# Kernel optimization log

Measured on AMD Instinct MI355X. Metric: run time of the kernel, lower is better.

## Reference

```python
import jax, jax.numpy as jnp
import numpy as np

ITERS = 8
LAMBDA0 = 0.01
PAD = 1.0
LR = 1.0
EPS = 1e-12


def _sobel_grads(fmap):
    # kornia spatial_gradient: normalized 3x3 sobel (/8), replicate padding. fmap: C,H,W
    kx = jnp.array([[-1., 0., 1.], [-2., 0., 2.], [-1., 0., 1.]], fmap.dtype) / 8.0
    k = jnp.stack([kx, kx.T])[:, None]                       # 2,1,3,3 (OIHW)
    f = jnp.pad(fmap, ((0, 0), (1, 1), (1, 1)), mode='edge')[:, None]  # C,1,H+2,W+2
    g = jax.lax.conv_general_dilated(f, k, (1, 1), 'VALID')  # C,2,H,W
    return g[:, 0], g[:, 1]


def _bilinear(tensor, pts):
    # grid_sample bilinear, align_corners=True, at pixel coords. tensor: C,H,W; pts: N,2 (x,y) -> N,C
    c, h, w = tensor.shape
    x, y = pts[:, 0], pts[:, 1]
    x0 = jnp.clip(jnp.floor(x), 0, w - 1)
    y0 = jnp.clip(jnp.floor(y), 0, h - 1)
    x1 = jnp.clip(x0 + 1, 0, w - 1)
    y1 = jnp.clip(y0 + 1, 0, h - 1)
    wx, wy = x - x0, y - y0
    x0i, x1i = x0.astype(jnp.int32), x1.astype(jnp.int32)
    y0i, y1i = y0.astype(jnp.int32), y1.astype(jnp.int32)
    v00 = tensor[:, y0i, x0i]
    v01 = tensor[:, y0i, x1i]
    v10 = tensor[:, y1i, x0i]
    v11 = tensor[:, y1i, x1i]
    out = (v00 * (1 - wx) * (1 - wy) + v01 * wx * (1 - wy)
           + v10 * (1 - wx) * wy + v11 * wx * wy)
    return out.T


def _skew(v):
    x, y, z = v[..., 0], v[..., 1], v[..., 2]
    o = jnp.zeros_like(x)
    return jnp.stack([o, -z, y, z, o, -x, -y, x, o], -1).reshape(v.shape[:-1] + (3, 3))


def _so3exp(w):
    theta = jnp.linalg.norm(w)
    small = theta < 1e-7
    th = jnp.where(small, 1.0, theta)
    A = jnp.where(small, 1.0, jnp.sin(th) / th)
    B = jnp.where(small, 0.5, (1.0 - jnp.cos(th)) / th ** 2)
    W = _skew(w)
    return jnp.eye(3, dtype=w.dtype) + A * W + B * (W @ W)


def _normalize(x):
    return x / jnp.maximum(jnp.linalg.norm(x, axis=-1, keepdims=True), EPS)


def _pnp(p3D, feature_ref, feature_query, K, R_init, t_init):
    C, H, W = feature_query.shape
    gx, gy = _sobel_grads(feature_query)
    fref = _normalize(feature_ref)
    fx, fy, cx, cy = K[0, 0], K[1, 1], K[0, 2], K[1, 2]
    f_scale = jnp.stack([fx, fy])
    c_off = jnp.stack([cx, cy])

    def project(R, t):
        p3q = p3D @ R.T + t
        pn = p3q[:, :2] / p3q[:, 2:3]
        return p3q, pn, pn * f_scale + c_off

    def in_image(p2):
        return ((p2[:, 0] >= PAD) & (p2[:, 0] < W - PAD)
                & (p2[:, 1] >= PAD) & (p2[:, 1] < H - PAD))

    def masked_cost(p2, vf):
        f = _normalize(_bilinear(feature_query, p2))
        cost = ((f - fref) ** 2).sum(-1)
        return (cost * vf).sum() / vf.sum()

    R, t = R_init, t_init
    lam = jnp.asarray(LAMBDA0, p3D.dtype)
    jacobi = None
    cost_best = None
    p2D_init = None

    for i in range(ITERS):
        p3q, pn, p2 = project(R, t)
        if i == 0:
            p2D_init = jax.lax.stop_gradient(p2)
        vf = in_image(p2).astype(p3D.dtype)  # mask-weight == gather of valid pts

        f_raw = _bilinear(feature_query, p2)  # N,C
        norm = jnp.maximum(jnp.linalg.norm(f_raw, axis=-1, keepdims=True), EPS)
        f = f_raw / norm
        error = f - fref
        if i == 0:
            cost_best = (((error ** 2).sum(-1)) * vf).sum() / vf.sum()

        # Jacobian chain: J = J_f_p2 @ J_p2_pn @ J_pn_p3 @ J_p3_T   -> N,C,6
        x_, y_, d = p3q[:, 0], p3q[:, 1], p3q[:, 2]
        z = jnp.zeros_like(d)
        Jpn = jnp.stack([1 / d, z, -x_ / d ** 2,
                         z, 1 / d, -y_ / d ** 2], -1).reshape(-1, 2, 3)
        Jpn = Jpn * f_scale[None, :, None]  # fold in J_p2_pn = diag(fx,fy)
        Jp3T = jnp.concatenate(
            [jnp.broadcast_to(jnp.eye(3, dtype=p3D.dtype), p3q.shape[:-1] + (3, 3)),
             -_skew(p3q)], -1)  # N,3,6
        J26 = Jpn @ Jp3T       # N,2,6

        Jf = jnp.stack([_bilinear(gx, p2), _bilinear(gy, p2)], -1)  # N,C,2
        # normalize-feat Jacobian (I - f f^T)/||f_raw||, fused (no NxCxC)
        proj = jnp.einsum('nc,nck->nk', f, Jf)
        Jf = (Jf - f[:, :, None] * proj[:, None, :]) / norm[:, :, None]

        J = Jf @ J26  # N,C,6
        if i == 0:
            jacobi = 1.0 / (1.0 + jnp.linalg.norm(J * vf[:, None, None], axis=(0, 1)))
        J = J * jacobi

        Grad = jnp.einsum('ncj,nc,n->j', J, error, vf)
        Hess = jnp.einsum('nci,ncj,n->ij', J, J, vf)

        damp = jnp.diag(jnp.diagonal(Hess) + 1e-9) * lam  # LM damping
        delta = -LR * jnp.linalg.solve(Hess + damp, Grad)
        delta = delta * jacobi
        dt, dw = delta[:3], delta[3:6]
        dr = _so3exp(dw)
        R_new, t_new = dr @ R, dr @ t + dt

        _, _, p2_new = project(R_new, t_new)
        vf_new = in_image(p2_new).astype(p3D.dtype)
        cost_new = masked_cost(p2_new, vf_new)

        accept = cost_new <= cost_best
        lam = jnp.clip(lam * jnp.where(accept, 0.1, 10.0), 1e-8, 1e4)
        R = jnp.where(accept, R_new, R)
        t = jnp.where(accept, t_new, t)
        cost_best = jnp.where(accept, cost_new, cost_best)

    p3D_sg = jax.lax.stop_gradient(p3D)
    pf = p3D_sg @ R.T + t
    p2f = (pf[:, :2] / pf[:, 2:3]) * f_scale + c_off
    f_i = _normalize(_bilinear(feature_query, p2D_init))
    f_f = _normalize(_bilinear(feature_query, p2f))
    cost_init = ((fref - f_i) ** 2).sum(-1)
    cost_final = ((fref - f_f) ** 2).sum(-1)
    nan = jnp.asarray(jnp.nan, cost_init.dtype)
    cost_init = jnp.where(in_image(p2D_init), cost_init, nan)
    cost_final = jnp.where(in_image(p2f), cost_final, nan)
    return R, t, cost_init, cost_final


def setup_inputs() -> dict:
    N, C, H, W = 10000, 128, 512, 512
    key = jax.random.key(0)
    ks = jax.random.split(key, 4)
    xy = jax.random.uniform(ks[0], (N, 2), jnp.float32, -2.0, 2.0)
    z = jax.random.uniform(ks[1], (N, 1), jnp.float32, 4.0, 10.0)
    p3D = jnp.concatenate([xy, z], -1)
    feature_query = jax.random.normal(ks[2], (C, H, W), jnp.float32) * 0.5
    feature_ref = jax.random.normal(ks[3], (N, C), jnp.float32)
    K = jnp.array([[500., 0., 256.], [0., 500., 256.], [0., 0., 1.]], jnp.float32)
    R_init = _so3exp(jnp.array([0.01, -0.02, 0.015], jnp.float32))
    t_init = jnp.array([0.05, -0.03, 0.10], jnp.float32)
    return {"p3D": p3D, "feature_ref": feature_ref, "feature_query": feature_query,
            "K": K, "R_init": R_init, "t_init": t_init}


def reference(p3D, feature_ref, feature_query, K, R_init, t_init):
    return _pnp(p3D, feature_ref, feature_query, K, R_init, t_init)
```

## Files before the change

### kernel.cpp

```cpp
#include <hip/hip_runtime.h>
#include <hip/hip_fp16.h>
#include <math.h>

#define HW_ (512*512)
#define CSTRIDE 32

typedef float vf4 __attribute__((ext_vector_type(4)));

__device__ __forceinline__ float wred(float v){
#pragma unroll
  for (int o = 32; o > 0; o >>= 1) v += __shfl_xor(v, o, 64);
  return v;
}

template<bool TR>
__device__ __forceinline__ float2 tap(const void* __restrict__ f, int y, int x, int c0){
  if (TR){
    const __half2* p = (const __half2*)f + (((size_t)((y << 9) + x)) << 6) + (c0 >> 1);
    return __half22float2(*p);
  } else {
    const float* ff = (const float*)f;
    int base = (y << 9) + x;
    float2 r;
    r.x = ff[(size_t)c0 * HW_ + base];
    r.y = ff[(size_t)(c0 + 1) * HW_ + base];
    return r;
  }
}

__device__ __forceinline__ void fgrad(const float P[16], float w00, float w01, float w10, float w11,
                                      float& f, float& gx, float& gy){
  f = w00*P[5] + w01*P[6] + w10*P[9] + w11*P[10];
  float gx11 = (P[2]  + 2.f*P[6]  + P[10] - P[0] - 2.f*P[4]  - P[8] ) * 0.125f;
  float gx12 = (P[3]  + 2.f*P[7]  + P[11] - P[1] - 2.f*P[5]  - P[9] ) * 0.125f;
  float gx21 = (P[6]  + 2.f*P[10] + P[14] - P[4] - 2.f*P[8]  - P[12]) * 0.125f;
  float gx22 = (P[7]  + 2.f*P[11] + P[15] - P[5] - 2.f*P[9]  - P[13]) * 0.125f;
  gx = w00*gx11 + w01*gx12 + w10*gx21 + w11*gx22;
  float gy11 = (P[8]  + 2.f*P[9]  + P[10] - P[0] - 2.f*P[1]  - P[2] ) * 0.125f;
  float gy12 = (P[9]  + 2.f*P[10] + P[11] - P[1] - 2.f*P[2]  - P[3] ) * 0.125f;
  float gy21 = (P[12] + 2.f*P[13] + P[14] - P[4] - 2.f*P[5]  - P[6] ) * 0.125f;
  float gy22 = (P[13] + 2.f*P[14] + P[15] - P[5] - 2.f*P[6]  - P[7] ) * 0.125f;
  gy = w00*gy11 + w01*gy12 + w10*gy21 + w11*gy22;
}

template<bool TR>
__device__ __forceinline__ float cost_point_raw(const void* __restrict__ fmap,
                                                const float* __restrict__ fref,
                                                int n, float px, float py, int lane){
  int c0 = 2 * lane;
  float x0f = fminf(fmaxf(floorf(px), 0.f), 511.f);
  float y0f = fminf(fmaxf(floorf(py), 0.f), 511.f);
  int x0 = (int)x0f, y0 = (int)y0f;
  int x1 = min(x0 + 1, 511), y1 = min(y0 + 1, 511);
  float wx = px - x0f, wy = py - y0f;
  float w00 = (1.f-wx)*(1.f-wy), w01 = wx*(1.f-wy), w10 = (1.f-wx)*wy, w11 = wx*wy;
  float2 a = tap<TR>(fmap, y0, x0, c0), b = tap<TR>(fmap, y0, x1, c0);
  float2 c = tap<TR>(fmap, y1, x0, c0), d = tap<TR>(fmap, y1, x1, c0);
  float f0 = w00*a.x + w01*b.x + w10*c.x + w11*d.x;
  float f1 = w00*a.y + w01*b.y + w10*c.y + w11*d.y;
  const float2 fr = *(const float2*)(fref + (size_t)n*128 + c0);
  float Sff  = wred(f0*f0 + f1*f1);
  float Sffr = wred(f0*fr.x + f1*fr.y);
  float Sfr  = wred(fr.x*fr.x + fr.y*fr.y);
  float inv = 1.f / fmaxf(sqrtf(Sff), 1e-12f);
  float irn = 1.f / fmaxf(sqrtf(Sfr), 1e-12f);
  return Sff*inv*inv - 2.f*Sffr*inv*irn + Sfr*irn*irn;
}

__global__ __launch_bounds__(512) void transpose_kernel(const float* __restrict__ fq,
                                                        __half* __restrict__ ftr,
                                                        double* __restrict__ cur2){
  __shared__ __half tile[256 * 128];
  int t = threadIdx.x;
  if (blockIdx.x == 0 && t < 32) cur2[t * CSTRIDE] = 0.0;
  int sb = blockIdx.x << 8;
  int l = t & 63, r = t >> 6;
  int px0 = l << 2;
#pragma unroll
  for (int p = 0; p < 16; p++){
    int ch = p * 8 + r;
    vf4 v = __builtin_nontemporal_load((const vf4*)(fq + (size_t)ch * HW_ + sb + px0));
#pragma unroll
    for (int j = 0; j < 4; j++){
      int px = px0 + j;
      tile[px * 128 + (ch ^ (px & 0x78))] = __float2half(v[j]);
    }
  }
  __syncthreads();
#pragma unroll
  for (int p = 0; p < 8; p++){
    int px = p * 32 + (t >> 4);
    int c8 = (t & 15) << 3;
    int cs = c8 ^ (px & 0x78);
    uint4 v = *(const uint4*)&tile[px * 128 + cs];
    *(uint4*)(ftr + ((size_t)(sb + px) << 7) + c8) = v;
  }
}

__global__ void init_kernel(double* __restrict__ cur2){
  if (threadIdx.x < 32) cur2[threadIdx.x * CSTRIDE] = 0.0;
}

template<bool TR>
__device__ __forceinline__ bool gather_pt(
    const float* __restrict__ p3D, const float* __restrict__ fref,
    const void* __restrict__ fmap, const float* Rl, const float* Tl,
    float fx, float fy, float cx, float cy,
    int n, int lane, float s[10], float& X, float& Y, float& D)
{
  float PX = p3D[3*n], PY = p3D[3*n+1], PZ = p3D[3*n+2];
  X = Rl[0]*PX + Rl[1]*PY + Rl[2]*PZ + Tl[0];
  Y = Rl[3]*PX + Rl[4]*PY + Rl[5]*PZ + Tl[1];
  D = Rl[6]*PX + Rl[7]*PY + Rl[8]*PZ + Tl[2];
  float px = X / D * fx + cx;
  float py = Y / D * fy + cy;
  if (!(px >= 1.f && px < 511.f && py >= 1.f && py < 511.f)) return false;
  int c0 = 2 * lane;
  float x0f = fminf(fmaxf(floorf(px), 0.f), 511.f);
  float y0f = fminf(fmaxf(floorf(py), 0.f), 511.f);
  int x0 = (int)x0f, y0 = (int)y0f;
  int x1 = min(x0 + 1, 511), y1 = min(y0 + 1, 511);
  float wx = px - x0f, wy = py - y0f;
  int xs[4] = {max(x0-1,0), x0, x1, min(x1+1,511)};
  int ys[4] = {max(y0-1,0), y0, y1, min(y1+1,511)};
  float Pa[16], Pb[16];
#pragma unroll
  for (int rr = 0; rr < 4; rr++)
#pragma unroll
    for (int sc = 0; sc < 4; sc++){
      float2 v = tap<TR>(fmap, ys[rr], xs[sc], c0);
      Pa[rr*4+sc] = v.x; Pb[rr*4+sc] = v.y;
    }
  float w00 = (1.f-wx)*(1.f-wy), w01 = wx*(1.f-wy), w10 = (1.f-wx)*wy, w11 = wx*wy;
  float f0, gx0, gy0, f1, gx1, gy1;
  fgrad(Pa, w00, w01, w10, w11, f0, gx0, gy0);
  fgrad(Pb, w00, w01, w10, w11, f1, gx1, gy1);
  const float2 fr = *(const float2*)(fref + (size_t)n*128 + c0);
  s[0] = f0*f0 + f1*f1;
  s[1] = f0*fr.x + f1*fr.y;
  s[2] = fr.x*fr.x + fr.y*fr.y;
  s[3] = f0*gx0 + f1*gx1;
  s[4] = f0*gy0 + f1*gy1;
  s[5] = gx0*fr.x + gx1*fr.y;
  s[6] = gy0*fr.x + gy1*fr.y;
  s[7] = gx0*gx0 + gx1*gx1;
  s[8] = gx0*gy0 + gx1*gy1;
  s[9] = gy0*gy0 + gy1*gy1;
  return true;
}

__device__ __forceinline__ float slot_val(const float s[10], float X, float Y, float D,
                                          float fx, float fy, int lane, int li, int lj,
                                          float& se2)
{
  float inv = 1.f / fmaxf(sqrtf(s[0]), 1e-12f);
  float irn = 1.f / fmaxf(sqrtf(s[2]), 1e-12f);
  float inv2 = inv*inv, inv3 = inv2*inv, inv4 = inv2*inv2;
  float Sffr = s[1]*irn, Sgxfr = s[5]*irn, Sgyfr = s[6]*irn, Sfr = s[2]*irn*irn;
  se2 = s[0]*inv2 - 2.f*Sffr*inv + Sfr;
  float gex = s[3]*inv2 - Sgxfr*inv - s[3]*s[0]*inv4 + s[3]*Sffr*inv3;
  float gey = s[4]*inv2 - Sgyfr*inv - s[4]*s[0]*inv4 + s[4]*Sffr*inv3;
  float sxx = s[7]*inv2 - s[3]*s[3]*inv4;
  float sxy = s[8]*inv2 - s[3]*s[4]*inv4;
  float syy = s[9]*inv2 - s[4]*s[4]*inv4;
  float invD = 1.f / D;
  float rx = X * invD, ry = Y * invD;
  float A[6] = {fx*invD, 0.f, -fx*rx*invD, -fx*rx*ry, fx*(1.f+rx*rx), -fx*ry};
  float B[6] = {0.f, fy*invD, -fy*ry*invD, -fy*(1.f+ry*ry), fy*rx*ry, fy*rx};
  float val = 0.f;
  if (lane < 6)        val = A[lane]*gex + B[lane]*gey;
  else if (lane < 27)  val = A[li]*A[lj]*sxx + (A[li]*B[lj] + A[lj]*B[li])*sxy + B[li]*B[lj]*syy;
  else if (lane == 27) val = se2;
  else if (lane == 28) val = 1.f;
  return val;
}

template<bool TR>
__global__ __launch_bounds__(512) void eval_kernel(
    const float* __restrict__ p3D, const float* __restrict__ fref,
    const void* __restrict__ fmap, const float* __restrict__ Km,
    const float* __restrict__ Rm, const float* __restrict__ tm,
    double* __restrict__ cur2, float* __restrict__ cost_out, int N)
{
  int t = threadIdx.x;
  int lane = t & 63;
  int wv = t >> 6;
  int gw = blockIdx.x * 8 + wv;
  int n0 = gw * 2, n1 = n0 + 1;
  float fx = Km[0], fy = Km[4], cx = Km[2], cy = Km[5];
  float Rl[9], Tl[3];
#pragma unroll
  for (int i = 0; i < 9; i++) Rl[i] = Rm[i];
#pragma unroll
  for (int i = 0; i < 3; i++) Tl[i] = tm[i];
  int li = 0, lj = 0;
  {
    const int pi_[21] = {0,0,0,0,0,0,1,1,1,1,1,2,2,2,2,3,3,3,4,4,5};
    const int pj_[21] = {0,1,2,3,4,5,1,2,3,4,5,2,3,4,5,3,4,5,4,5,5};
    if (lane >= 6 && lane < 27){ li = pi_[lane-6]; lj = pj_[lane-6]; }
  }
  float sA[10], sB[10];
  float XA=0, YA=0, DA=1, XB=0, YB=0, DB=1;
  bool vA = false, vB = false;
  if (n0 < N) vA = gather_pt<TR>(p3D, fref, fmap, Rl, Tl, fx, fy, cx, cy, n0, lane, sA, XA, YA, DA);
  if (n1 < N) vB = gather_pt<TR>(p3D, fref, fmap, Rl, Tl, fx, fy, cx, cy, n1, lane, sB, XB, YB, DB);
  if (vA){
#pragma unroll
    for (int i = 0; i < 10; i++) sA[i] = wred(sA[i]);
  }
  if (vB){
#pragma unroll
    for (int i = 0; i < 10; i++) sB[i] = wred(sB[i]);
  }
  double acc = 0.0;
  float se2A = 0.f, se2B = 0.f;
  if (vA) acc += (double)slot_val(sA, XA, YA, DA, fx, fy, lane, li, lj, se2A);
  if (vB) acc += (double)slot_val(sB, XB, YB, DB, fx, fy, lane, li, lj, se2B);
  if (cost_out && lane == 0){
    const float nanv = __int_as_float(0x7fc00000);
    if (n0 < N) cost_out[n0] = vA ? se2A : nanv;
    if (n1 < N) cost_out[n1] = vB ? se2B : nanv;
  }
  __shared__ double red[8][32];
  if (lane < 32) red[wv][lane] = acc;
  __syncthreads();
  if (t < 32){
    double ssum = 0.0;
#pragma unroll
    for (int i = 0; i < 8; i++) ssum += red[i][t];
    if (ssum != 0.0) atomicAdd(&cur2[t * CSTRIDE], ssum);
  }
}

template<bool TR>
__global__ __launch_bounds__(512) void cost_kernel(
    const float* __restrict__ p3D, const float* __restrict__ fref,
    const void* __restrict__ fmap, const float* __restrict__ Km,
    const float* __restrict__ Rm, const float* __restrict__ tm,
    double* __restrict__ cur2, int N)
{
  int t = threadIdx.x;
  int lane = t & 63;
  int wv = t >> 6;
  int gw = blockIdx.x * 8 + wv;
  int n0 = gw * 2, n1 = n0 + 1;
  float fx = Km[0], fy = Km[4], cx = Km[2], cy = Km[5];
  float Rl[9], Tl[3];
#pragma unroll
  for (int i = 0; i < 9; i++) Rl[i] = Rm[i];
#pragma unroll
  for (int i = 0; i < 3; i++) Tl[i] = tm[i];
  double accc = 0.0, accn = 0.0;
#pragma unroll
  for (int q = 0; q < 2; q++){
    int n = q ? n1 : n0;
    if (n >= N) continue;
    float PX = p3D[3*n], PY = p3D[3*n+1], PZ = p3D[3*n+2];
    float X = Rl[0]*PX + Rl[1]*PY + Rl[2]*PZ + Tl[0];
    float Y = Rl[3]*PX + Rl[4]*PY + Rl[5]*PZ + Tl[1];
    float D = Rl[6]*PX + Rl[7]*PY + Rl[8]*PZ + Tl[2];
    float px = X / D * fx + cx, py = Y / D * fy + cy;
    if (px >= 1.f && px < 511.f && py >= 1.f && py < 511.f){
      float cp = cost_point_raw<TR>(fmap, fref, n, px, py, lane);
      accc += (double)cp; accn += 1.0;
    }
  }
  double acc = (lane == 27) ? accc : ((lane == 28) ? accn : 0.0);
  __shared__ double red[8][32];
  if (lane < 32) red[wv][lane] = acc;
  __syncthreads();
  if (t < 32){
    double ssum = 0.0;
#pragma unroll
    for (int i = 0; i < 8; i++) ssum += red[i][t];
    if (ssum != 0.0) atomicAdd(&cur2[t * CSTRIDE], ssum);
  }
}

__device__ void solve_step(const double* __restrict__ cur, float* __restrict__ state){
  const int pi_[21] = {0,0,0,0,0,0,1,1,1,1,1,2,2,2,2,3,3,3,4,4,5};
  const int pj_[21] = {0,1,2,3,4,5,1,2,3,4,5,2,3,4,5,3,4,5,4,5,5};
  double rg[6]; for (int i = 0; i < 6; i++) rg[i] = cur[i];
  double rh[6][6];
  for (int k = 0; k < 21; k++){ rh[pi_[k]][pj_[k]] = cur[6+k]; rh[pj_[k]][pi_[k]] = cur[6+k]; }
  float jac[6];
  for (int j = 0; j < 6; j++) jac[j] = state[24+j];
  double lam = (double)state[30];
  double H[6][7];
  for (int i = 0; i < 6; i++)
    for (int j = 0; j < 6; j++) H[i][j] = (double)jac[i] * (double)jac[j] * rh[i][j];
  for (int i = 0; i < 6; i++) H[i][i] += (H[i][i] + 1e-9) * lam;
  for (int i = 0; i < 6; i++) H[i][6] = -((double)jac[i] * rg[i]);
  for (int k = 0; k < 6; k++){
    int p = k; double mx = fabs(H[k][k]);
    for (int r = k+1; r < 6; r++) if (fabs(H[r][k]) > mx){ mx = fabs(H[r][k]); p = r; }
    if (p != k) for (int c = k; c < 7; c++){ double tmp = H[k][c]; H[k][c] = H[p][c]; H[p][c] = tmp; }
    double inv = 1.0 / H[k][k];
    for (int r = k+1; r < 6; r++){
      double m = H[r][k] * inv;
      for (int c = k; c < 7; c++) H[r][c] -= m * H[k][c];
    }
  }
  double d[6];
  for (int i = 5; i >= 0; i--){
    double sx = H[i][6];
    for (int c = i+1; c < 6; c++) sx -= H[i][c] * d[c];
    d[i] = sx / H[i][i];
  }
  for (int j = 0; j < 6; j++) d[j] *= (double)jac[j];
  double wx = d[3], wy = d[4], wz = d[5];
  double th2 = wx*wx + wy*wy + wz*wz, th = sqrt(th2);
  double Aa, Bb;
  if (th < 1e-7){ Aa = 1.0; Bb = 0.5; } else { Aa = sin(th)/th; Bb = (1.0 - cos(th))/th2; }
  double W[3][3] = {{0,-wz,wy},{wz,0,-wx},{-wy,wx,0}};
  double W2[3][3];
  for (int i = 0; i < 3; i++) for (int j = 0; j < 3; j++){
    double q = 0; for (int k = 0; k < 3; k++) q += W[i][k]*W[k][j]; W2[i][j] = q;
  }
  double dr[3][3];
  for (int i = 0; i < 3; i++) for (int j = 0; j < 3; j++)
    dr[i][j] = (i == j ? 1.0 : 0.0) + Aa*W[i][j] + Bb*W2[i][j];
  double Rc[3][3], tc[3];
  for (int i = 0; i < 3; i++){ tc[i] = state[9+i]; for (int j = 0; j < 3; j++) Rc[i][j] = state[i*3+j]; }
  for (int i = 0; i < 3; i++){
    for (int j = 0; j < 3; j++){
      double q = 0; for (int k = 0; k < 3; k++) q += dr[i][k]*Rc[k][j];
      state[12 + i*3 + j] = (float)q;
    }
    double q = 0; for (int k = 0; k < 3; k++) q += dr[i][k]*tc[k];
    state[21 + i] = (float)(q + d[i]);
  }
}

__global__ void update_kernel(double* __restrict__ cur2, float* __restrict__ state,
                              double* __restrict__ cur,
                              const float* __restrict__ Rin, const float* __restrict__ tin,
                              int iter)
{
  if (threadIdx.x != 0) return;
  double tot[32];
  for (int i = 0; i < 32; i++){ tot[i] = cur2[i * CSTRIDE]; cur2[i * CSTRIDE] = 0.0; }
  if (iter < 0){
    for (int i = 0; i < 9; i++) state[i] = Rin[i];
    for (int i = 0; i < 3; i++) state[9+i] = tin[i];
    state[30] = 0.01f;
    const int diag_k[6] = {0, 6, 11, 15, 18, 20};
    for (int j = 0; j < 6; j++)
      state[24+j] = 1.0f / (1.0f + (float)sqrt(tot[6 + diag_k[j]]));
    state[31] = (float)(tot[27] / tot[28]);
    for (int k = 0; k < 32; k++) cur[k] = tot[k];
    solve_step(cur, state);
  } else {
    float cn = (float)(tot[27] / tot[28]);
    bool acpt = (cn <= state[31]);
    float lam = state[30] * (acpt ? 0.1f : 10.f);
    state[30] = fminf(fmaxf(lam, 1e-8f), 1e4f);
    if (acpt){
      for (int i = 0; i < 12; i++) state[i] = state[12+i];
      state[31] = cn;
      for (int k = 0; k < 32; k++) cur[k] = tot[k];
    }
    if (iter < 7) solve_step(cur, state);
  }
}

template<bool TR>
__global__ __launch_bounds__(256) void final_kernel(
    const float* __restrict__ p3D, const float* __restrict__ fref,
    const void* __restrict__ fmap, const float* __restrict__ Km,
    const float* __restrict__ state, float* __restrict__ out, int N)
{
  if (blockIdx.x == 0 && threadIdx.x < 12) out[threadIdx.x] = state[threadIdx.x];
  int lane = threadIdx.x & 63;
  int n = blockIdx.x * 4 + (threadIdx.x >> 6);
  if (n >= N) return;
  float fx = Km[0], fy = Km[4], cx = Km[2], cy = Km[5];
  float PX = p3D[3*n], PY = p3D[3*n+1], PZ = p3D[3*n+2];
  float X = state[0]*PX + state[1]*PY + state[2]*PZ + state[9];
  float Y = state[3]*PX + state[4]*PY + state[5]*PZ + state[10];
  float D = state[6]*PX + state[7]*PY + state[8]*PZ + state[11];
  float px = X / D * fx + cx, py = Y / D * fy + cy;
  bool vf = (px >= 1.f && px < 511.f && py >= 1.f && py < 511.f);
  float cf = __int_as_float(0x7fc00000);
  if (vf) cf = cost_point_raw<TR>(fmap, fref, n, px, py, lane);
  if (lane == 0) out[12 + N + n] = cf;
}

extern "C" void kernel_launch(void* const* d_in, const int* in_sizes, int n_in,
                              void* d_out, int out_size, void* d_ws, size_t ws_size,
                              hipStream_t stream)
{
  const float* p3D  = (const float*)d_in[0];
  const float* fref = (const float*)d_in[1];
  const float* fq   = (const float*)d_in[2];
  const float* Km   = (const float*)d_in[3];
  const float* Rin  = (const float*)d_in[4];
  const float* tin  = (const float*)d_in[5];
  float* out = (float*)d_out;
  int N = in_sizes[0] / 3;
  int NEB   = (N + 15) / 16;
  int NBLK4 = (N + 3) / 4;

  char* w = (char*)d_ws;
  float*  state = (float*)w;
  double* cur   = (double*)(w + 256);
  double* cur2  = (double*)(w + 512);
  size_t ftr_off = (512 + 32 * CSTRIDE * 8 + 255) & ~(size_t)255;
  __half* ftr = (__half*)(w + ftr_off);
  size_t need = ftr_off + (size_t)HW_ * 128 * 2;
  bool tr = (ws_size >= need);

  if (tr) transpose_kernel<<<HW_/256, 512, 0, stream>>>(fq, ftr, cur2);
  else    init_kernel<<<1, 64, 0, stream>>>(cur2);
  const void* fmap = tr ? (const void*)ftr : (const void*)fq;

  if (tr) eval_kernel<true ><<<NEB, 512, 0, stream>>>(p3D, fref, fmap, Km, Rin, tin, cur2, out + 12, N);
  else    eval_kernel<false><<<NEB, 512, 0, stream>>>(p3D, fref, fmap, Km, Rin, tin, cur2, out + 12, N);
  update_kernel<<<1, 64, 0, stream>>>(cur2, state, cur, Rin, tin, -1);

  for (int it = 0; it < 7; it++){
    if (tr) eval_kernel<true ><<<NEB, 512, 0, stream>>>(p3D, fref, fmap, Km, state + 12, state + 21, cur2, nullptr, N);
    else    eval_kernel<false><<<NEB, 512, 0, stream>>>(p3D, fref, fmap, Km, state + 12, state + 21, cur2, nullptr, N);
    update_kernel<<<1, 64, 0, stream>>>(cur2, state, cur, Rin, tin, it);
  }
  if (tr) cost_kernel<true ><<<NEB, 512, 0, stream>>>(p3D, fref, fmap, Km, state + 12, state + 21, cur2, N);
  else    cost_kernel<false><<<NEB, 512, 0, stream>>>(p3D, fref, fmap, Km, state + 12, state + 21, cur2, N);
  update_kernel<<<1, 64, 0, stream>>>(cur2, state, cur, Rin, tin, 7);

  if (tr) final_kernel<true ><<<NBLK4, 256, 0, stream>>>(p3D, fref, fmap, Km, state, out, N);
  else    final_kernel<false><<<NBLK4, 256, 0, stream>>>(p3D, fref, fmap, Km, state, out, N);
}
```

Before: 485.5 us.

## Cache per-point costs across LM iterations and restructure eval into persistent grid-stride

Per-point costs from each trial pose are kept in a workspace buffer and copied into the final-cost output when the update accepts a step. This removes the final kernel's re-gather of the feature map, which now only copies cached values. Eval and cost kernels switch to a fixed 1024-block grid-stride loop with 256-thread blocks and one point per wave per pass. The atomic accumulators are spread over 8 slots per quantity and summed in the update kernel. The sobel/bilinear gather is also restructured to stream one row of taps at a time with folded weights, which lowers register pressure at the cost of more logic coupling the kernels through state[32].

```diff
diff --git a/kernel.cpp b/kernel.cpp
--- a/kernel.cpp
+++ b/kernel.cpp
@@ -3,7 +3,6 @@
 #include <math.h>
 
 #define HW_ (512*512)
-#define CSTRIDE 32
 
 typedef float vf4 __attribute__((ext_vector_type(4)));
 
@@ -26,21 +25,6 @@
     r.y = ff[(size_t)(c0 + 1) * HW_ + base];
     return r;
   }
-}
-
-__device__ __forceinline__ void fgrad(const float P[16], float w00, float w01, float w10, float w11,
-                                      float& f, float& gx, float& gy){
-  f = w00*P[5] + w01*P[6] + w10*P[9] + w11*P[10];
-  float gx11 = (P[2]  + 2.f*P[6]  + P[10] - P[0] - 2.f*P[4]  - P[8] ) * 0.125f;
-  float gx12 = (P[3]  + 2.f*P[7]  + P[11] - P[1] - 2.f*P[5]  - P[9] ) * 0.125f;
-  float gx21 = (P[6]  + 2.f*P[10] + P[14] - P[4] - 2.f*P[8]  - P[12]) * 0.125f;
-  float gx22 = (P[7]  + 2.f*P[11] + P[15] - P[5] - 2.f*P[9]  - P[13]) * 0.125f;
-  gx = w00*gx11 + w01*gx12 + w10*gx21 + w11*gx22;
-  float gy11 = (P[8]  + 2.f*P[9]  + P[10] - P[0] - 2.f*P[1]  - P[2] ) * 0.125f;
-  float gy12 = (P[9]  + 2.f*P[10] + P[11] - P[1] - 2.f*P[2]  - P[3] ) * 0.125f;
-  float gy21 = (P[12] + 2.f*P[13] + P[14] - P[4] - 2.f*P[5]  - P[6] ) * 0.125f;
-  float gy22 = (P[13] + 2.f*P[14] + P[15] - P[5] - 2.f*P[6]  - P[7] ) * 0.125f;
-  gy = w00*gy11 + w01*gy12 + w10*gy21 + w11*gy22;
 }
 
 template<bool TR>
@@ -72,7 +56,7 @@
                                                         double* __restrict__ cur2){
   __shared__ __half tile[256 * 128];
   int t = threadIdx.x;
-  if (blockIdx.x == 0 && t < 32) cur2[t * CSTRIDE] = 0.0;
+  if (blockIdx.x == 0 && t < 256) cur2[t] = 0.0;
   int sb = blockIdx.x << 8;
   int l = t & 63, r = t >> 6;
   int px0 = l << 2;
@@ -98,7 +82,7 @@
 }
 
 __global__ void init_kernel(double* __restrict__ cur2){
-  if (threadIdx.x < 32) cur2[threadIdx.x * CSTRIDE] = 0.0;
+  if (threadIdx.x < 256) cur2[threadIdx.x] = 0.0;
 }
 
 template<bool TR>
@@ -121,20 +105,42 @@
   int x0 = (int)x0f, y0 = (int)y0f;
   int x1 = min(x0 + 1, 511), y1 = min(y0 + 1, 511);
   float wx = px - x0f, wy = py - y0f;
-  int xs[4] = {max(x0-1,0), x0, x1, min(x1+1,511)};
-  int ys[4] = {max(y0-1,0), y0, y1, min(y1+1,511)};
-  float Pa[16], Pb[16];
-#pragma unroll
-  for (int rr = 0; rr < 4; rr++)
-#pragma unroll
-    for (int sc = 0; sc < 4; sc++){
-      float2 v = tap<TR>(fmap, ys[rr], xs[sc], c0);
-      Pa[rr*4+sc] = v.x; Pb[rr*4+sc] = v.y;
-    }
-  float w00 = (1.f-wx)*(1.f-wy), w01 = wx*(1.f-wy), w10 = (1.f-wx)*wy, w11 = wx*wy;
-  float f0, gx0, gy0, f1, gx1, gy1;
-  fgrad(Pa, w00, w01, w10, w11, f0, gx0, gy0);
-  fgrad(Pb, w00, w01, w10, w11, f1, gx1, gy1);
+  int xs0 = max(x0-1,0), xs3 = min(x1+1,511);
+  int ys0 = max(y0-1,0), ys3 = min(y1+1,511);
+  float ea = (1.f-wx)*(1.f-wy), eb = wx*(1.f-wy), ec = (1.f-wx)*wy, ed = wx*wy;
+  float a8 = 0.125f*ea, b8 = 0.125f*eb, c8 = 0.125f*ec, d8 = 0.125f*ed;
+  float gL1 = 2.f*a8 + c8, gR1 = 2.f*b8 + d8;
+  float gL2 = a8 + 2.f*c8, gR2 = b8 + 2.f*d8;
+  float ya0 = a8, ya1 = 2.f*a8 + b8, ya2 = a8 + 2.f*b8, ya3 = b8;
+  float yc0 = c8, yc1 = 2.f*c8 + d8, yc2 = c8 + 2.f*d8, yc3 = d8;
+  float f0=0.f, f1=0.f, gx0=0.f, gx1=0.f, gy0=0.f, gy1=0.f;
+  float2 t0, t1, t2, t3;
+  t0 = tap<TR>(fmap, ys0, xs0, c0); t1 = tap<TR>(fmap, ys0, x0, c0);
+  t2 = tap<TR>(fmap, ys0, x1,  c0); t3 = tap<TR>(fmap, ys0, xs3, c0);
+  gx0 += a8*(t2.x-t0.x) + b8*(t3.x-t1.x);
+  gx1 += a8*(t2.y-t0.y) + b8*(t3.y-t1.y);
+  gy0 -= ya0*t0.x + ya1*t1.x + ya2*t2.x + ya3*t3.x;
+  gy1 -= ya0*t0.y + ya1*t1.y + ya2*t2.y + ya3*t3.y;
+  t0 = tap<TR>(fmap, y0, xs0, c0); t1 = tap<TR>(fmap, y0, x0, c0);
+  t2 = tap<TR>(fmap, y0, x1,  c0); t3 = tap<TR>(fmap, y0, xs3, c0);
+  gx0 += gL1*(t2.x-t0.x) + gR1*(t3.x-t1.x);
+  gx1 += gL1*(t2.y-t0.y) + gR1*(t3.y-t1.y);
+  gy0 -= yc0*t0.x + yc1*t1.x + yc2*t2.x + yc3*t3.x;
+  gy1 -= yc0*t0.y + yc1*t1.y + yc2*t2.y + yc3*t3.y;
+  f0 += ea*t1.x + eb*t2.x;  f1 += ea*t1.y + eb*t2.y;
+  t0 = tap<TR>(fmap, y1, xs0, c0); t1 = tap<TR>(fmap, y1, x0, c0);
+  t2 = tap<TR>(fmap, y1, x1,  c0); t3 = tap<TR>(fmap, y1, xs3, c0);
+  gx0 += gL2*(t2.x-t0.x) + gR2*(t3.x-t1.x);
+  gx1 += gL2*(t2.y-t0.y) + gR2*(t3.y-t1.y);
+  gy0 += ya0*t0.x + ya1*t1.x + ya2*t2.x + ya3*t3.x;
+  gy1 += ya0*t0.y + ya1*t1.y + ya2*t2.y + ya3*t3.y;
+  f0 += ec*t1.x + ed*t2.x;  f1 += ec*t1.y + ed*t2.y;
+  t0 = tap<TR>(fmap, ys3, xs0, c0); t1 = tap<TR>(fmap, ys3, x0, c0);
+  t2 = tap<TR>(fmap, ys3, x1,  c0); t3 = tap<TR>(fmap, ys3, xs3, c0);
+  gx0 += c8*(t2.x-t0.x) + d8*(t3.x-t1.x);
+  gx1 += c8*(t2.y-t0.y) + d8*(t3.y-t1.y);
+  gy0 += yc0*t0.x + yc1*t1.x + yc2*t2.x + yc3*t3.x;
+  gy1 += yc0*t0.y + yc1*t1.y + yc2*t2.y + yc3*t3.y;
   const float2 fr = *(const float2*)(fref + (size_t)n*128 + c0);
   s[0] = f0*f0 + f1*f1;
   s[1] = f0*fr.x + f1*fr.y;
@@ -176,17 +182,21 @@
 }
 
 template<bool TR>
-__global__ __launch_bounds__(512) void eval_kernel(
+__global__ __launch_bounds__(256) void eval_kernel(
     const float* __restrict__ p3D, const float* __restrict__ fref,
     const void* __restrict__ fmap, const float* __restrict__ Km,
     const float* __restrict__ Rm, const float* __restrict__ tm,
-    double* __restrict__ cur2, float* __restrict__ cost_out, int N)
-{
-  int t = threadIdx.x;
-  int lane = t & 63;
-  int wv = t >> 6;
-  int gw = blockIdx.x * 8 + wv;
-  int n0 = gw * 2, n1 = n0 + 1;
+    const float* __restrict__ state, double* __restrict__ cur2,
+    float* __restrict__ costT, float* __restrict__ costF,
+    float* __restrict__ costI, int N, int mode)
+{
+  int t = threadIdx.x, lane = t & 63, wv = t >> 6;
+  int gw = blockIdx.x * 4 + wv;
+  int nw = (gridDim.x * blockDim.x) >> 6;
+  if (mode == 1 && state[32] != 0.f){
+    int nn = gw + lane * nw;
+    if (lane < 4 && nn < N) costF[nn] = costT[nn];
+  }
   float fx = Km[0], fy = Km[4], cx = Km[2], cy = Km[5];
   float Rl[9], Tl[3];
 #pragma unroll
@@ -199,81 +209,73 @@
     const int pj_[21] = {0,1,2,3,4,5,1,2,3,4,5,2,3,4,5,3,4,5,4,5,5};
     if (lane >= 6 && lane < 27){ li = pi_[lane-6]; lj = pj_[lane-6]; }
   }
-  float sA[10], sB[10];
-  float XA=0, YA=0, DA=1, XB=0, YB=0, DB=1;
-  bool vA = false, vB = false;
-  if (n0 < N) vA = gather_pt<TR>(p3D, fref, fmap, Rl, Tl, fx, fy, cx, cy, n0, lane, sA, XA, YA, DA);
-  if (n1 < N) vB = gather_pt<TR>(p3D, fref, fmap, Rl, Tl, fx, fy, cx, cy, n1, lane, sB, XB, YB, DB);
-  if (vA){
-#pragma unroll
-    for (int i = 0; i < 10; i++) sA[i] = wred(sA[i]);
-  }
-  if (vB){
-#pragma unroll
-    for (int i = 0; i < 10; i++) sB[i] = wred(sB[i]);
-  }
+  const float nanv = __int_as_float(0x7fc00000);
   double acc = 0.0;
-  float se2A = 0.f, se2B = 0.f;
-  if (vA) acc += (double)slot_val(sA, XA, YA, DA, fx, fy, lane, li, lj, se2A);
-  if (vB) acc += (double)slot_val(sB, XB, YB, DB, fx, fy, lane, li, lj, se2B);
-  if (cost_out && lane == 0){
-    const float nanv = __int_as_float(0x7fc00000);
-    if (n0 < N) cost_out[n0] = vA ? se2A : nanv;
-    if (n1 < N) cost_out[n1] = vB ? se2B : nanv;
-  }
-  __shared__ double red[8][32];
+  for (int n = gw; n < N; n += nw){
+    float s[10], X, Y, D;
+    bool v = gather_pt<TR>(p3D, fref, fmap, Rl, Tl, fx, fy, cx, cy, n, lane, s, X, Y, D);
+    float se2 = 0.f;
+    if (v){
+#pragma unroll
+      for (int i = 0; i < 10; i++) s[i] = wred(s[i]);
+      acc += (double)slot_val(s, X, Y, D, fx, fy, lane, li, lj, se2);
+    }
+    if (lane == 0){
+      float cv = v ? se2 : nanv;
+      if (mode == 0){ costI[n] = cv; costF[n] = cv; }
+      else costT[n] = cv;
+    }
+  }
+  __shared__ double red[4][32];
   if (lane < 32) red[wv][lane] = acc;
   __syncthreads();
   if (t < 32){
-    double ssum = 0.0;
-#pragma unroll
-    for (int i = 0; i < 8; i++) ssum += red[i][t];
-    if (ssum != 0.0) atomicAdd(&cur2[t * CSTRIDE], ssum);
+    double ssum = red[0][t] + red[1][t] + red[2][t] + red[3][t];
+    if (ssum != 0.0) atomicAdd(&cur2[t*8 + (blockIdx.x & 7)], ssum);
   }
 }
 
 template<bool TR>
-__global__ __launch_bounds__(512) void cost_kernel(
+__global__ __launch_bounds__(256) void cost_kernel(
     const float* __restrict__ p3D, const float* __restrict__ fref,
     const void* __restrict__ fmap, const float* __restrict__ Km,
     const float* __restrict__ Rm, const float* __restrict__ tm,
-    double* __restrict__ cur2, int N)
-{
-  int t = threadIdx.x;
-  int lane = t & 63;
-  int wv = t >> 6;
-  int gw = blockIdx.x * 8 + wv;
-  int n0 = gw * 2, n1 = n0 + 1;
+    const float* __restrict__ state, double* __restrict__ cur2,
+    float* __restrict__ costT, float* __restrict__ costF, int N)
+{
+  int t = threadIdx.x, lane = t & 63, wv = t >> 6;
+  int gw = blockIdx.x * 4 + wv;
+  int nw = (gridDim.x * blockDim.x) >> 6;
+  if (state[32] != 0.f){
+    int nn = gw + lane * nw;
+    if (lane < 4 && nn < N) costF[nn] = costT[nn];
+  }
   float fx = Km[0], fy = Km[4], cx = Km[2], cy = Km[5];
   float Rl[9], Tl[3];
 #pragma unroll
   for (int i = 0; i < 9; i++) Rl[i] = Rm[i];
 #pragma unroll
   for (int i = 0; i < 3; i++) Tl[i] = tm[i];
+  const float nanv = __int_as_float(0x7fc00000);
   double accc = 0.0, accn = 0.0;
-#pragma unroll
-  for (int q = 0; q < 2; q++){
-    int n = q ? n1 : n0;
-    if (n >= N) continue;
+  for (int n = gw; n < N; n += nw){
     float PX = p3D[3*n], PY = p3D[3*n+1], PZ = p3D[3*n+2];
     float X = Rl[0]*PX + Rl[1]*PY + Rl[2]*PZ + Tl[0];
     float Y = Rl[3]*PX + Rl[4]*PY + Rl[5]*PZ + Tl[1];
     float D = Rl[6]*PX + Rl[7]*PY + Rl[8]*PZ + Tl[2];
     float px = X / D * fx + cx, py = Y / D * fy + cy;
-    if (px >= 1.f && px < 511.f && py >= 1.f && py < 511.f){
-      float cp = cost_point_raw<TR>(fmap, fref, n, px, py, lane);
-      accc += (double)cp; accn += 1.0;
-    }
+    bool v = (px >= 1.f && px < 511.f && py >= 1.f && py < 511.f);
+    float cp = 0.f;
+    if (v){ cp = cost_point_raw<TR>(fmap, fref, n, px, py, lane); accc += (double)cp; accn += 1.0; }
+    if (lane == 0) costT[n] = v ? cp : nanv;
   }
   double acc = (lane == 27) ? accc : ((lane == 28) ? accn : 0.0);
-  __shared__ double red[8][32];
+  __shared__ double red[4][32];
   if (lane < 32) red[wv][lane] = acc;
   __syncthreads();
   if (t < 32){
-    double ssum = 0.0;
-#pragma unroll
-    for (int i = 0; i < 8; i++) ssum += red[i][t];
-    if (ssum != 0.0) atomicAdd(&cur2[t * CSTRIDE], ssum);
+    double ssum = red[0][t] + red[1][t] + red[2][t] + red[3][t];
+    if (ssum != 0.0) atomicAdd(&cur2[t*8 + (blockIdx.x & 7)], ssum);
   }
 }
 
@@ -337,13 +339,21 @@
                               const float* __restrict__ Rin, const float* __restrict__ tin,
                               int iter)
 {
-  if (threadIdx.x != 0) return;
-  double tot[32];
-  for (int i = 0; i < 32; i++){ tot[i] = cur2[i * CSTRIDE]; cur2[i * CSTRIDE] = 0.0; }
+  __shared__ double tot[32];
+  int t = threadIdx.x;
+  if (t < 32){
+    double s = 0.0;
+#pragma unroll
+    for (int k = 0; k < 8; k++){ s += cur2[t*8 + k]; cur2[t*8 + k] = 0.0; }
+    tot[t] = s;
+  }
+  __syncthreads();
+  if (t != 0) return;
   if (iter < 0){
     for (int i = 0; i < 9; i++) state[i] = Rin[i];
     for (int i = 0; i < 3; i++) state[9+i] = tin[i];
     state[30] = 0.01f;
+    state[32] = 0.f;
     const int diag_k[6] = {0, 6, 11, 15, 18, 20};
     for (int j = 0; j < 6; j++)
       state[24+j] = 1.0f / (1.0f + (float)sqrt(tot[6 + diag_k[j]]));
@@ -355,6 +365,7 @@
     bool acpt = (cn <= state[31]);
     float lam = state[30] * (acpt ? 0.1f : 10.f);
     state[30] = fminf(fmaxf(lam, 1e-8f), 1e4f);
+    state[32] = acpt ? 1.f : 0.f;
     if (acpt){
       for (int i = 0; i < 12; i++) state[i] = state[12+i];
       state[31] = cn;
@@ -364,26 +375,16 @@
   }
 }
 
-template<bool TR>
-__global__ __launch_bounds__(256) void final_kernel(
-    const float* __restrict__ p3D, const float* __restrict__ fref,
-    const void* __restrict__ fmap, const float* __restrict__ Km,
-    const float* __restrict__ state, float* __restrict__ out, int N)
-{
-  if (blockIdx.x == 0 && threadIdx.x < 12) out[threadIdx.x] = state[threadIdx.x];
-  int lane = threadIdx.x & 63;
-  int n = blockIdx.x * 4 + (threadIdx.x >> 6);
-  if (n >= N) return;
-  float fx = Km[0], fy = Km[4], cx = Km[2], cy = Km[5];
-  float PX = p3D[3*n], PY = p3D[3*n+1], PZ = p3D[3*n+2];
-  float X = state[0]*PX + state[1]*PY + state[2]*PZ + state[9];
-  float Y = state[3]*PX + state[4]*PY + state[5]*PZ + state[10];
-  float D = state[6]*PX + state[7]*PY + state[8]*PZ + state[11];
-  float px = X / D * fx + cx, py = Y / D * fy + cy;
-  bool vf = (px >= 1.f && px < 511.f && py >= 1.f && py < 511.f);
-  float cf = __int_as_float(0x7fc00000);
-  if (vf) cf = cost_point_raw<TR>(fmap, fref, n, px, py, lane);
-  if (lane == 0) out[12 + N + n] = cf;
+__global__ __launch_bounds__(256) void final_kernel(const float* __restrict__ state,
+                                                    const float* __restrict__ costT,
+                                                    float* __restrict__ out, int N)
+{
+  int g = blockIdx.x * blockDim.x + threadIdx.x;
+  if (g < 12) out[g] = state[g];
+  if (state[32] != 0.f){
+    int stride = gridDim.x * blockDim.x;
+    for (int n = g; n < N; n += stride) out[12 + N + n] = costT[n];
+  }
 }
 
 extern "C" void kernel_launch(void* const* d_in, const int* in_sizes, int n_in,
@@ -398,35 +399,37 @@
   const float* tin  = (const float*)d_in[5];
   float* out = (float*)d_out;
   int N = in_sizes[0] / 3;
-  int NEB   = (N + 15) / 16;
-  int NBLK4 = (N + 3) / 4;
+  const int EBLK = 1024;
 
   char* w = (char*)d_ws;
   float*  state = (float*)w;
   double* cur   = (double*)(w + 256);
   double* cur2  = (double*)(w + 512);
-  size_t ftr_off = (512 + 32 * CSTRIDE * 8 + 255) & ~(size_t)255;
+  float*  costT = (float*)(w + 2560);
+  size_t ftr_off = (2560 + (size_t)N*4 + 255) & ~(size_t)255;
   __half* ftr = (__half*)(w + ftr_off);
   size_t need = ftr_off + (size_t)HW_ * 128 * 2;
   bool tr = (ws_size >= need);
 
+  float* costI = out + 12;
+  float* costF = out + 12 + N;
+
   if (tr) transpose_kernel<<<HW_/256, 512, 0, stream>>>(fq, ftr, cur2);
-  else    init_kernel<<<1, 64, 0, stream>>>(cur2);
+  else    init_kernel<<<1, 256, 0, stream>>>(cur2);
   const void* fmap = tr ? (const void*)ftr : (const void*)fq;
 
-  if (tr) eval_kernel<true ><<<NEB, 512, 0, stream>>>(p3D, fref, fmap, Km, Rin, tin, cur2, out + 12, N);
-  else    eval_kernel<false><<<NEB, 512, 0, stream>>>(p3D, fref, fmap, Km, Rin, tin, cur2, out + 12, N);
+  if (tr) eval_kernel<true ><<<EBLK, 256, 0, stream>>>(p3D, fref, fmap, Km, Rin, tin, state, cur2, costT, costF, costI, N, 0);
+  else    eval_kernel<false><<<EBLK, 256, 0, stream>>>(p3D, fref, fmap, Km, Rin, tin, state, cur2, costT, costF, costI, N, 0);
   update_kernel<<<1, 64, 0, stream>>>(cur2, state, cur, Rin, tin, -1);
 
   for (int it = 0; it < 7; it++){
-    if (tr) eval_kernel<true ><<<NEB, 512, 0, stream>>>(p3D, fref, fmap, Km, state + 12, state + 21, cur2, nullptr, N);
-    else    eval_kernel<false><<<NEB, 512, 0, stream>>>(p3D, fref, fmap, Km, state + 12, state + 21, cur2, nullptr, N);
+    if (tr) eval_kernel<true ><<<EBLK, 256, 0, stream>>>(p3D, fref, fmap, Km, state + 12, state + 21, state, cur2, costT, costF, nullptr, N, 1);
+    else    eval_kernel<false><<<EBLK, 256, 0, stream>>>(p3D, fref, fmap, Km, state + 12, state + 21, state, cur2, costT, costF, nullptr, N, 1);
     update_kernel<<<1, 64, 0, stream>>>(cur2, state, cur, Rin, tin, it);
   }
-  if (tr) cost_kernel<true ><<<NEB, 512, 0, stream>>>(p3D, fref, fmap, Km, state + 12, state + 21, cur2, N);
-  else    cost_kernel<false><<<NEB, 512, 0, stream>>>(p3D, fref, fmap, Km, state + 12, state + 21, cur2, N);
+  if (tr) cost_kernel<true ><<<EBLK, 256, 0, stream>>>(p3D, fref, fmap, Km, state + 12, state + 21, state, cur2, costT, costF, N);
+  else    cost_kernel<false><<<EBLK, 256, 0, stream>>>(p3D, fref, fmap, Km, state + 12, state + 21, state, cur2, costT, costF, N);
   update_kernel<<<1, 64, 0, stream>>>(cur2, state, cur, Rin, tin, 7);
 
-  if (tr) final_kernel<true ><<<NBLK4, 256, 0, stream>>>(p3D, fref, fmap, Km, state, out, N);
-  else    final_kernel<false><<<NBLK4, 256, 0, stream>>>(p3D, fref, fmap, Km, state, out, N);
-}
+  final_kernel<<<256, 256, 0, stream>>>(state, costT, out, N);
+}
```

New measurement: 533.4 us. +9.9%, slower.
